# Kernel tuning notes

Measured on AMD Instinct MI355X. Metric: run time of the kernel, lower is better.

Reference implementation:

```python
import jax, jax.numpy as jnp
import numpy as np
import math

N_EMBD = 1024
N_HEAD = 16
D_FF = 4 * N_EMBD
B, T = 4, 2048

def gelu_tanh(x):
    return 0.5 * x * (1.0 + jnp.tanh(jnp.sqrt(2.0 / jnp.pi).astype(x.dtype) * (x + 0.044715 * x ** 3)))

def layernorm(x, g, b, eps=1e-5):
    mu = jnp.mean(x, axis=-1, keepdims=True)
    var = jnp.var(x, axis=-1, keepdims=True)
    return (x - mu) * jax.lax.rsqrt(var + eps) * g + b

def setup_inputs() -> dict:
    key = jax.random.key(0)
    ks = jax.random.split(key, 12)
    s = lambda fan_in: 1.0 / np.sqrt(fan_in)
    return {
        "x": jax.random.normal(ks[0], (B, T, N_EMBD), jnp.float32),
        "ln1_g": jnp.ones((N_EMBD,), jnp.float32),
        "ln1_b": jnp.zeros((N_EMBD,), jnp.float32),
        "w_attn": jax.random.normal(ks[1], (N_EMBD, 3 * N_EMBD), jnp.float32) * s(N_EMBD),
        "b_attn": jnp.zeros((3 * N_EMBD,), jnp.float32),
        "w_proj": jax.random.normal(ks[2], (N_EMBD, N_EMBD), jnp.float32) * s(N_EMBD),
        "b_proj": jnp.zeros((N_EMBD,), jnp.float32),
        "ln2_g": jnp.ones((N_EMBD,), jnp.float32),
        "ln2_b": jnp.zeros((N_EMBD,), jnp.float32),
        "w_fc": jax.random.normal(ks[3], (N_EMBD, D_FF), jnp.float32) * s(N_EMBD),
        "b_fc": jnp.zeros((D_FF,), jnp.float32),
        "w_fc2": jax.random.normal(ks[4], (D_FF, N_EMBD), jnp.float32) * s(D_FF),
        "b_fc2": jnp.zeros((N_EMBD,), jnp.float32),
    }

def reference(x, ln1_g, ln1_b, w_attn, b_attn, w_proj, b_proj,
              ln2_g, ln2_b, w_fc, b_fc, w_fc2, b_fc2):
    Bn, Tn, C = x.shape
    hs = C // N_HEAD
    # --- attention ---
    h = layernorm(x, ln1_g, ln1_b)
    qkv = h @ w_attn + b_attn  # [B,T,3C]
    q, k, v = jnp.split(qkv, 3, axis=-1)
    q = q.reshape(Bn, Tn, N_HEAD, hs).transpose(0, 2, 1, 3)
    k = k.reshape(Bn, Tn, N_HEAD, hs).transpose(0, 2, 1, 3)
    v = v.reshape(Bn, Tn, N_HEAD, hs).transpose(0, 2, 1, 3)
    att = jnp.einsum('bhqd,bhkd->bhqk', q, k) * (hs ** -0.5)
    mask = jnp.tril(jnp.ones((Tn, Tn), bool))
    att = jnp.where(mask, att, -jnp.inf)
    att = jax.nn.softmax(att, axis=-1)
    y = jnp.einsum('bhqk,bhkd->bhqd', att, v)
    y = y.transpose(0, 2, 1, 3).reshape(Bn, Tn, C)
    x = x + (y @ w_proj + b_proj)
    # --- MLP ---
    h2 = layernorm(x, ln2_g, ln2_b)
    h2 = gelu_tanh(h2 @ w_fc + b_fc)
    x = x + (h2 @ w_fc2 + b_fc2)
    return x
```

## Files before the change

kernel.cpp:

```cpp
#include <hip/hip_runtime.h>
#include <hip/hip_bf16.h>

#define B_ 4
#define T_ 2048
#define C_ 1024
#define NH_ 16
#define FF_ 4096
#define NT_ (B_*T_)

typedef short bf16x8 __attribute__((ext_vector_type(8)));
typedef float f32x4 __attribute__((ext_vector_type(4)));

#define LDS_AS(p) ((__attribute__((address_space(3))) uint32_t*)(p))
#define GLB_AS(p) ((const __attribute__((address_space(1))) uint32_t*)(p))

__device__ __forceinline__ float bf2f(__hip_bfloat16 v){ return __bfloat162float(v); }
__device__ __forceinline__ __hip_bfloat16 f2bf(float f){ return __float2bfloat16(f); }

__device__ __forceinline__ f32x4 mfma16(bf16x8 a, bf16x8 b, f32x4 c){
  return __builtin_amdgcn_mfma_f32_16x16x32_bf16(a, b, c, 0, 0, 0);
}

__global__ __launch_bounds__(256) void transpose_bf16(const float* __restrict__ in,
                                                      __hip_bfloat16* __restrict__ out,
                                                      int K, int N) {
  __shared__ float tile[32][33];
  const int n0 = blockIdx.x * 32, k0 = blockIdx.y * 32;
  const int x = threadIdx.x & 31, y = threadIdx.x >> 5;
  #pragma unroll
  for (int i = 0; i < 4; i++)
    tile[y + 8*i][x] = in[(size_t)(k0 + y + 8*i) * N + n0 + x];
  __syncthreads();
  #pragma unroll
  for (int i = 0; i < 4; i++)
    out[(size_t)(n0 + y + 8*i) * K + k0 + x] = f2bf(tile[x][y + 8*i]);
}

__global__ __launch_bounds__(256) void ln_bf16(const float* __restrict__ x,
                                               const float* __restrict__ g,
                                               const float* __restrict__ b,
                                               __hip_bfloat16* __restrict__ out) {
  const int row = blockIdx.x;
  const int tid = threadIdx.x;
  float4 v = ((const float4*)(x + (size_t)row * C_))[tid];
  float s  = v.x + v.y + v.z + v.w;
  float s2 = v.x*v.x + v.y*v.y + v.z*v.z + v.w*v.w;
  #pragma unroll
  for (int off = 32; off > 0; off >>= 1) {
    s  += __shfl_down(s,  off, 64);
    s2 += __shfl_down(s2, off, 64);
  }
  __shared__ float red[8];
  const int w = tid >> 6, l = tid & 63;
  if (l == 0) { red[w] = s; red[4 + w] = s2; }
  __syncthreads();
  s  = red[0] + red[1] + red[2] + red[3];
  s2 = red[4] + red[5] + red[6] + red[7];
  const float mu   = s * (1.0f / C_);
  const float var  = s2 * (1.0f / C_) - mu * mu;
  const float rstd = rsqrtf(var + 1e-5f);
  float4 gv = ((const float4*)g)[tid];
  float4 bv = ((const float4*)b)[tid];
  ushort4 o;
  __hip_bfloat16 t;
  t = f2bf((v.x - mu) * rstd * gv.x + bv.x); o.x = *(unsigned short*)&t;
  t = f2bf((v.y - mu) * rstd * gv.y + bv.y); o.y = *(unsigned short*)&t;
  t = f2bf((v.z - mu) * rstd * gv.z + bv.z); o.z = *(unsigned short*)&t;
  t = f2bf((v.w - mu) * rstd * gv.w + bv.w); o.w = *(unsigned short*)&t;
  ((ushort4*)out)[(size_t)row * (C_/4) + tid] = o;
}

template <int MODE>
__global__ __launch_bounds__(256) void gemm_bt(const __hip_bfloat16* __restrict__ A,
                                               const __hip_bfloat16* __restrict__ BT,
                                               const float* __restrict__ bias,
                                               const float* __restrict__ resid,
                                               void* __restrict__ outp,
                                               void* __restrict__ outp2,
                                               int N, int K) {
  __shared__ __hip_bfloat16 Als[128 * 64];
  __shared__ __hip_bfloat16 Bls[128 * 64];
  const int tid = threadIdx.x;
  const int w = tid >> 6, l = tid & 63;
  const int tile_n = blockIdx.x * 128;
  const int tile_m = blockIdx.y * 128;
  const int wm = (w >> 1) * 64, wn = (w & 1) * 64;

  f32x4 acc[4][4] = {};

  const int lrow8 = l >> 3;
  const int gchunk = (l & 7) ^ lrow8;
  const int m_ = (l & 15);
  const int q_ = (l >> 4);

  for (int k0 = 0; k0 < K; k0 += 64) {
    #pragma unroll
    for (int jj = 0; jj < 2; jj++) {
      const int r0 = w*16 + 8*jj + lrow8;
      __builtin_amdgcn_global_load_lds(GLB_AS(A  + (size_t)(tile_m + r0) * K + k0 + gchunk*8),
                                       LDS_AS(&Als[(w*16 + 8*jj) * 64]), 16, 0, 0);
      __builtin_amdgcn_global_load_lds(GLB_AS(A  + (size_t)(tile_m + 64 + r0) * K + k0 + gchunk*8),
                                       LDS_AS(&Als[(64 + w*16 + 8*jj) * 64]), 16, 0, 0);
      __builtin_amdgcn_global_load_lds(GLB_AS(BT + (size_t)(tile_n + r0) * K + k0 + gchunk*8),
                                       LDS_AS(&Bls[(w*16 + 8*jj) * 64]), 16, 0, 0);
      __builtin_amdgcn_global_load_lds(GLB_AS(BT + (size_t)(tile_n + 64 + r0) * K + k0 + gchunk*8),
                                       LDS_AS(&Bls[(64 + w*16 + 8*jj) * 64]), 16, 0, 0);
    }
    __syncthreads();
    bf16x8 af[2][4], bfr[2][4];
    #pragma unroll
    for (int c = 0; c < 2; c++) {
      #pragma unroll
      for (int mi = 0; mi < 4; mi++) {
        const int row = wm + mi*16 + m_;
        af[c][mi] = *(const bf16x8*)&Als[row * 64 + (((c*4 + q_) ^ (row & 7)) * 8)];
      }
      #pragma unroll
      for (int ni = 0; ni < 4; ni++) {
        const int row = wn + ni*16 + m_;
        bfr[c][ni] = *(const bf16x8*)&Bls[row * 64 + (((c*4 + q_) ^ (row & 7)) * 8)];
      }
    }
    #pragma unroll
    for (int c = 0; c < 2; c++)
      #pragma unroll
      for (int mi = 0; mi < 4; mi++)
        #pragma unroll
        for (int ni = 0; ni < 4; ni++)
          acc[mi][ni] = mfma16(af[c][mi], bfr[c][ni], acc[mi][ni]);
    __syncthreads();
  }

  const int r0 = tile_m + wm + q_ * 4;
  const int c0 = tile_n + wn + m_;
  #pragma unroll
  for (int mi = 0; mi < 4; mi++) {
    #pragma unroll
    for (int r = 0; r < 4; r++) {
      const int row = r0 + mi * 16 + r;
      #pragma unroll
      for (int ni = 0; ni < 4; ni++) {
        const int col = c0 + ni * 16;
        float v = acc[mi][ni][r] + bias[col];
        if (MODE == 0) {
          if (tile_n < 2 * C_) {
            ((__hip_bfloat16*)outp)[(size_t)row * (2*C_) + col] = f2bf(v);
          } else {
            const int dg = col - 2 * C_;
            ((__hip_bfloat16*)outp2)[((size_t)((row >> 11) * 1024 + dg)) * T_ + (row & 2047)] = f2bf(v);
          }
        } else if (MODE == 1 || MODE == 3) {
          ((float*)outp)[(size_t)row * N + col] = resid[(size_t)row * N + col] + v;
        } else {
          const float u = 0.7978845608028654f * (v + 0.044715f * v * v * v);
          const float e = __expf(2.0f * u);
          ((__hip_bfloat16*)outp)[(size_t)row * N + col] = f2bf(v * (1.0f - 1.0f / (e + 1.0f)));
        }
      }
    }
  }
}

__global__ __launch_bounds__(256, 2) void flash_attn(const __hip_bfloat16* __restrict__ qk,
                                                     const __hip_bfloat16* __restrict__ vT,
                                                     __hip_bfloat16* __restrict__ y) {
  const int id  = blockIdx.x;
  const int xcd = id & 7;
  const int jj  = id >> 3;
  const int bh  = xcd * 8 + (jj >> 3);
  const int p   = jj & 7;
  const int b   = bh >> 4, h = bh & 15;
  const int tid = threadIdx.x, w = tid >> 6, l = tid & 63;
  const int m_ = l & 15, q_ = l >> 4;

  __shared__ __hip_bfloat16 Pls[128 * 76];

  const size_t kgbase = (size_t)b * T_ * (2*C_) + C_ + h*64;
  const size_t vgbase = (size_t)bh * 64 * T_;

#define LOAD_KV(bkX, bvX, kt_) do {                                                   \
    _Pragma("unroll")                                                                 \
    for (int ni = 0; ni < 4; ni++) {                                                  \
      const __hip_bfloat16* kp = qk + kgbase + (size_t)((kt_)*64 + ni*16 + m_)*(2*C_);\
      union { uint4 u; bf16x8 f; } t0, t1;                                            \
      t0.u = *(const uint4*)(kp + q_*8);                                              \
      t1.u = *(const uint4*)(kp + 32 + q_*8);                                         \
      bkX[ni][0] = t0.f; bkX[ni][1] = t1.f;                                           \
    }                                                                                 \
    _Pragma("unroll")                                                                 \
    for (int ni = 0; ni < 4; ni++) {                                                  \
      const __hip_bfloat16* vp = vT + vgbase + (size_t)(ni*16 + m_)*T_ + (kt_)*64;    \
      union { uint4 u; bf16x8 f; } t2, t3;                                            \
      t2.u = *(const uint4*)(vp + q_*8);                                              \
      t3.u = *(const uint4*)(vp + 32 + q_*8);                                         \
      bvX[ni][0] = t2.f; bvX[ni][1] = t3.f;                                           \
    }                                                                                 \
  } while (0)

#define COMPUTE(bkX, bvX, kt_) do {                                                   \
    f32x4 s[2][4];                                                                    \
    _Pragma("unroll")                                                                 \
    for (int ni = 0; ni < 4; ni++)                                                    \
      _Pragma("unroll")                                                               \
      for (int mf = 0; mf < 2; mf++) {                                                \
        f32x4 z = {};                                                                 \
        z = mfma16(aq[mf][0], bkX[ni][0], z);                                         \
        s[mf][ni] = mfma16(aq[mf][1], bkX[ni][1], z);                                 \
      }                                                                               \
    if ((kt_) >= 2*qt) {                                                              \
      _Pragma("unroll")                                                               \
      for (int mf = 0; mf < 2; mf++) {                                                \
        const int qrow = q0 + w*32 + mf*16 + q_*4;                                    \
        _Pragma("unroll")                                                             \
        for (int ni = 0; ni < 4; ni++) {                                              \
          const int kcol = (kt_)*64 + ni*16 + m_;                                     \
          _Pragma("unroll")                                                           \
          for (int r = 0; r < 4; r++)                                                 \
            if (kcol > qrow + r) s[mf][ni][r] = -1e30f;                               \
        }                                                                             \
      }                                                                               \
    }                                                                                 \
    _Pragma("unroll")                                                                 \
    for (int mf = 0; mf < 2; mf++) {                                                  \
      _Pragma("unroll")                                                               \
      for (int ni = 0; ni < 4; ni++)                                                  \
        _Pragma("unroll")                                                             \
        for (int r = 0; r < 4; r++)                                                   \
          s[mf][ni][r] = exp2f(s[mf][ni][r]);                                         \
      _Pragma("unroll")                                                               \
      for (int r = 0; r < 4; r++)                                                     \
        lsum[mf][r] += (s[mf][0][r] + s[mf][1][r]) + (s[mf][2][r] + s[mf][3][r]);     \
      _Pragma("unroll")                                                               \
      for (int ni = 0; ni < 4; ni++)                                                  \
        _Pragma("unroll")                                                             \
        for (int r = 0; r < 4; r++)                                                   \
          Pls[(w*32 + mf*16 + q_*4 + r) * 76 + ni*16 + m_] = f2bf(s[mf][ni][r]);      \
    }                                                                                 \
    bf16x8 ap[2][2];                                                                  \
    _Pragma("unroll")                                                                 \
    for (int mf = 0; mf < 2; mf++) {                                                  \
      ap[mf][0] = *(const bf16x8*)&Pls[(w*32 + mf*16 + m_) * 76 + q_*8];              \
      ap[mf][1] = *(const bf16x8*)&Pls[(w*32 + mf*16 + m_) * 76 + 32 + q_*8];         \
    }                                                                                 \
    _Pragma("unroll")                                                                 \
    for (int ni = 0; ni < 4; ni++)                                                    \
      _Pragma("unroll")                                                               \
      for (int mf = 0; mf < 2; mf++) {                                                \
        accO[mf][ni] = mfma16(ap[mf][0], bvX[ni][0], accO[mf][ni]);                   \
        accO[mf][ni] = mfma16(ap[mf][1], bvX[ni][1], accO[mf][ni]);                   \
      }                                                                               \
  } while (0)

  #pragma unroll 1
  for (int ui = 0; ui < 2; ui++) {
    const int qt = ui ? (15 - p) : p;
    const int q0 = qt * 128;

    bf16x8 aq[2][2];
    {
      const float qscale = 0.125f * 1.44269504088896f;
      #pragma unroll
      for (int mf = 0; mf < 2; mf++) {
        const size_t qbase = ((size_t)b * T_ + q0 + w*32 + mf*16 + m_) * (2*C_) + h*64;
        #pragma unroll
        for (int kh = 0; kh < 2; kh++) {
          union { uint4 u; __hip_bfloat16 h8[8]; } t;
          t.u = *(const uint4*)&qk[qbase + kh*32 + q_*8];
          __hip_bfloat16 a[8];
          #pragma unroll
          for (int jx = 0; jx < 8; jx++) a[jx] = f2bf(bf2f(t.h8[jx]) * qscale);
          aq[mf][kh] = *(const bf16x8*)a;
        }
      }
    }

    f32x4 accO[2][4] = {};
    float lsum[2][4] = {{0.f,0.f,0.f,0.f},{0.f,0.f,0.f,0.f}};
    const int ktmax = 2*qt + 1;

    bf16x8 bkA[4][2], bvA[4][2], bkB[4][2], bvB[4][2];
    LOAD_KV(bkA, bvA, 0);
    for (int kt = 0; kt <= ktmax; kt += 2) {
      LOAD_KV(bkB, bvB, kt + 1);
      COMPUTE(bkA, bvA, kt);
      if (kt + 2 <= ktmax) LOAD_KV(bkA, bvA, kt + 2);
      COMPUTE(bkB, bvB, kt + 1);
    }

    #pragma unroll
    for (int mf = 0; mf < 2; mf++)
      #pragma unroll
      for (int r = 0; r < 4; r++) {
        #pragma unroll
        for (int d = 1; d < 16; d <<= 1)
          lsum[mf][r] += __shfl_xor(lsum[mf][r], d, 64);
      }

    const size_t ybase = ((size_t)b * T_ + q0) * C_ + h*64;
    #pragma unroll
    for (int mf = 0; mf < 2; mf++) {
      #pragma unroll
      for (int r = 0; r < 4; r++) {
        const int row = w*32 + mf*16 + q_*4 + r;
        const float linv = 1.0f / lsum[mf][r];
        #pragma unroll
        for (int ni = 0; ni < 4; ni++)
          y[ybase + (size_t)row * C_ + ni*16 + m_] = f2bf(accO[mf][ni][r] * linv);
      }
    }
  }
#undef LOAD_KV
#undef COMPUTE
}

extern "C" void kernel_launch(void* const* d_in, const int* in_sizes, int n_in,
                              void* d_out, int out_size, void* d_ws, size_t ws_size,
                              hipStream_t stream) {
  const float* x      = (const float*)d_in[0];
  const float* ln1_g  = (const float*)d_in[1];
  const float* ln1_b  = (const float*)d_in[2];
  const float* w_attn = (const float*)d_in[3];
  const float* b_attn = (const float*)d_in[4];
  const float* w_proj = (const float*)d_in[5];
  const float* b_proj = (const float*)d_in[6];
  const float* ln2_g  = (const float*)d_in[7];
  const float* ln2_b  = (const float*)d_in[8];
  const float* w_fc   = (const float*)d_in[9];
  const float* b_fc   = (const float*)d_in[10];
  const float* w_fc2  = (const float*)d_in[11];
  const float* b_fc2  = (const float*)d_in[12];
  float* out = (float*)d_out;

  char* ws = (char*)d_ws;
  const size_t MB = 1024 * 1024;
  __hip_bfloat16* h      = (__hip_bfloat16*)(ws);
  __hip_bfloat16* qk     = (__hip_bfloat16*)(ws + 16*MB);
  __hip_bfloat16* vT     = (__hip_bfloat16*)(ws + 48*MB);
  __hip_bfloat16* y      = (__hip_bfloat16*)(ws + 64*MB);
  float*          x2     = (float*)        (ws + 80*MB);
  __hip_bfloat16* h2     = (__hip_bfloat16*)(ws + 64*MB);
  __hip_bfloat16* gbuf   = (__hip_bfloat16*)(ws);
  __hip_bfloat16* wattnT = (__hip_bfloat16*)(ws + 112*MB);
  __hip_bfloat16* wprojT = (__hip_bfloat16*)(ws + 118*MB);
  __hip_bfloat16* wfcT   = (__hip_bfloat16*)(ws + 120*MB);
  __hip_bfloat16* wfc2T  = (__hip_bfloat16*)(ws + 128*MB);

  transpose_bf16<<<dim3(3*C_/32, C_/32), 256, 0, stream>>>(w_attn, wattnT, C_, 3*C_);
  transpose_bf16<<<dim3(C_/32,  C_/32), 256, 0, stream>>>(w_proj, wprojT, C_, C_);
  transpose_bf16<<<dim3(FF_/32, C_/32), 256, 0, stream>>>(w_fc,   wfcT,   C_, FF_);
  transpose_bf16<<<dim3(C_/32, FF_/32), 256, 0, stream>>>(w_fc2,  wfc2T,  FF_, C_);

  ln_bf16<<<NT_, 256, 0, stream>>>(x, ln1_g, ln1_b, h);
  gemm_bt<0><<<dim3(3*C_/128, NT_/128), 256, 0, stream>>>(h, wattnT, b_attn, nullptr, qk, vT, 3*C_, C_);
  flash_attn<<<dim3(512), 256, 0, stream>>>(qk, vT, y);
  gemm_bt<1><<<dim3(C_/128, NT_/128), 256, 0, stream>>>(y, wprojT, b_proj, x, x2, nullptr, C_, C_);
  ln_bf16<<<NT_, 256, 0, stream>>>(x2, ln2_g, ln2_b, h2);
  gemm_bt<2><<<dim3(FF_/128, NT_/128), 256, 0, stream>>>(h2, wfcT, b_fc, nullptr, gbuf, nullptr, FF_, C_);
  gemm_bt<3><<<dim3(C_/128, NT_/128), 256, 0, stream>>>(gbuf, wfc2T, b_fc2, x2, out, nullptr, C_, FF_);
}
```

Baseline: 609.2 us.

## Remap GEMM tiles per XCD and trim flash-attn V register buffering

GEMM launches switch to a 1D grid whose block ids are remapped so each XCD owns a contiguous band of N-columns across all M tiles. The intent is better L2 reuse of the weight tiles within each XCD. Flash attention drops double buffering of V to a single buffer loaded just before each compute step, and lowers the launch-bounds occupancy hint to 1. This frees registers but exposes V load latency and may reduce occupancy.

```diff
diff --git a/kernel.cpp b/kernel.cpp
--- a/kernel.cpp
+++ b/kernel.cpp
@@ -82,8 +82,12 @@
   __shared__ __hip_bfloat16 Bls[128 * 64];
   const int tid = threadIdx.x;
   const int w = tid >> 6, l = tid & 63;
-  const int tile_n = blockIdx.x * 128;
-  const int tile_m = blockIdx.y * 128;
+  const int id = blockIdx.x;
+  const int xcd = id & 7;
+  const int rr = id >> 3;
+  const int nPerX = (N >> 7) >> 3;
+  const int tile_n = (xcd * nPerX + (rr >> 6)) * 128;
+  const int tile_m = (rr & 63) * 128;
   const int wm = (w >> 1) * 64, wn = (w & 1) * 64;
 
   f32x4 acc[4][4] = {};
@@ -161,7 +165,7 @@
   }
 }
 
-__global__ __launch_bounds__(256, 2) void flash_attn(const __hip_bfloat16* __restrict__ qk,
+__global__ __launch_bounds__(256, 1) void flash_attn(const __hip_bfloat16* __restrict__ qk,
                                                      const __hip_bfloat16* __restrict__ vT,
                                                      __hip_bfloat16* __restrict__ y) {
   const int id  = blockIdx.x;
@@ -178,7 +182,7 @@
   const size_t kgbase = (size_t)b * T_ * (2*C_) + C_ + h*64;
   const size_t vgbase = (size_t)bh * 64 * T_;
 
-#define LOAD_KV(bkX, bvX, kt_) do {                                                   \
+#define LOAD_K(bkX, kt_) do {                                                         \
     _Pragma("unroll")                                                                 \
     for (int ni = 0; ni < 4; ni++) {                                                  \
       const __hip_bfloat16* kp = qk + kgbase + (size_t)((kt_)*64 + ni*16 + m_)*(2*C_);\
@@ -187,17 +191,20 @@
       t1.u = *(const uint4*)(kp + 32 + q_*8);                                         \
       bkX[ni][0] = t0.f; bkX[ni][1] = t1.f;                                           \
     }                                                                                 \
+  } while (0)
+
+#define LOAD_V(kt_) do {                                                              \
     _Pragma("unroll")                                                                 \
     for (int ni = 0; ni < 4; ni++) {                                                  \
       const __hip_bfloat16* vp = vT + vgbase + (size_t)(ni*16 + m_)*T_ + (kt_)*64;    \
       union { uint4 u; bf16x8 f; } t2, t3;                                            \
       t2.u = *(const uint4*)(vp + q_*8);                                              \
       t3.u = *(const uint4*)(vp + 32 + q_*8);                                         \
-      bvX[ni][0] = t2.f; bvX[ni][1] = t3.f;                                           \
+      bv[ni][0] = t2.f; bv[ni][1] = t3.f;                                             \
     }                                                                                 \
   } while (0)
 
-#define COMPUTE(bkX, bvX, kt_) do {                                                   \
+#define COMPUTE(bkX, kt_) do {                                                        \
     f32x4 s[2][4];                                                                    \
     _Pragma("unroll")                                                                 \
     for (int ni = 0; ni < 4; ni++)                                                    \
@@ -246,8 +253,8 @@
     for (int ni = 0; ni < 4; ni++)                                                    \
       _Pragma("unroll")                                                               \
       for (int mf = 0; mf < 2; mf++) {                                                \
-        accO[mf][ni] = mfma16(ap[mf][0], bvX[ni][0], accO[mf][ni]);                   \
-        accO[mf][ni] = mfma16(ap[mf][1], bvX[ni][1], accO[mf][ni]);                   \
+        accO[mf][ni] = mfma16(ap[mf][0], bv[ni][0], accO[mf][ni]);                    \
+        accO[mf][ni] = mfma16(ap[mf][1], bv[ni][1], accO[mf][ni]);                    \
       }                                                                               \
   } while (0)
 
@@ -278,13 +285,15 @@
     float lsum[2][4] = {{0.f,0.f,0.f,0.f},{0.f,0.f,0.f,0.f}};
     const int ktmax = 2*qt + 1;
 
-    bf16x8 bkA[4][2], bvA[4][2], bkB[4][2], bvB[4][2];
-    LOAD_KV(bkA, bvA, 0);
+    bf16x8 bkA[4][2], bkB[4][2], bv[4][2];
+    LOAD_K(bkA, 0);
     for (int kt = 0; kt <= ktmax; kt += 2) {
-      LOAD_KV(bkB, bvB, kt + 1);
-      COMPUTE(bkA, bvA, kt);
-      if (kt + 2 <= ktmax) LOAD_KV(bkA, bvA, kt + 2);
-      COMPUTE(bkB, bvB, kt + 1);
+      LOAD_V(kt);
+      LOAD_K(bkB, kt + 1);
+      COMPUTE(bkA, kt);
+      LOAD_V(kt + 1);
+      if (kt + 2 <= ktmax) LOAD_K(bkA, kt + 2);
+      COMPUTE(bkB, kt + 1);
     }
 
     #pragma unroll
@@ -309,7 +318,8 @@
       }
     }
   }
-#undef LOAD_KV
+#undef LOAD_K
+#undef LOAD_V
 #undef COMPUTE
 }
 
@@ -351,10 +361,10 @@
   transpose_bf16<<<dim3(C_/32, FF_/32), 256, 0, stream>>>(w_fc2,  wfc2T,  FF_, C_);
 
   ln_bf16<<<NT_, 256, 0, stream>>>(x, ln1_g, ln1_b, h);
-  gemm_bt<0><<<dim3(3*C_/128, NT_/128), 256, 0, stream>>>(h, wattnT, b_attn, nullptr, qk, vT, 3*C_, C_);
+  gemm_bt<0><<<dim3((3*C_/128) * 64), 256, 0, stream>>>(h, wattnT, b_attn, nullptr, qk, vT, 3*C_, C_);
   flash_attn<<<dim3(512), 256, 0, stream>>>(qk, vT, y);
-  gemm_bt<1><<<dim3(C_/128, NT_/128), 256, 0, stream>>>(y, wprojT, b_proj, x, x2, nullptr, C_, C_);
+  gemm_bt<1><<<dim3((C_/128) * 64), 256, 0, stream>>>(y, wprojT, b_proj, x, x2, nullptr, C_, C_);
   ln_bf16<<<NT_, 256, 0, stream>>>(x2, ln2_g, ln2_b, h2);
-  gemm_bt<2><<<dim3(FF_/128, NT_/128), 256, 0, stream>>>(h2, wfcT, b_fc, nullptr, gbuf, nullptr, FF_, C_);
-  gemm_bt<3><<<dim3(C_/128, NT_/128), 256, 0, stream>>>(gbuf, wfc2T, b_fc2, x2, out, nullptr, C_, FF_);
-}
+  gemm_bt<2><<<dim3((FF_/128) * 64), 256, 0, stream>>>(h2, wfcT, b_fc, nullptr, gbuf, nullptr, FF_, C_);
+  gemm_bt<3><<<dim3((C_/128) * 64), 256, 0, stream>>>(gbuf, wfc2T, b_fc2, x2, out, nullptr, C_, FF_);
+}
```

New measurement: 628.6 us. +3.2%, slower.
